# Kernel tuning notes

Hardware: AMD Instinct MI355X
Metric: run time of the kernel (lower is better)

The kernel has to match this reference:

```python
import jax, jax.numpy as jnp
from jax import lax
import numpy as np

THRESHOLD = 1.25
CURRENT_DECAY = 0.25
VOLTAGE_DECAY = 0.03
TAU_GRAD = 0.03
SCALE_GRAD = 3.0


@jax.custom_vjp
def spike_fn(v):
    # Heaviside spike on membrane voltage (threshold already subtracted)
    return (v >= 0.0).astype(v.dtype)

def _spike_fwd(v):
    return spike_fn(v), v

def _spike_bwd(v, g):
    # slayer-style exponential surrogate gradient around threshold
    surrogate = SCALE_GRAD * jnp.exp(-jnp.abs(v) / TAU_GRAD)
    return (g * surrogate,)

spike_fn.defvjp(_spike_fwd, _spike_bwd)


def cuba_dense(x, v_w, g_w, delay):
    """x: [B, C_in, T] spikes -> [B, C_out, T] spikes.
    Weight-normalized dense synapse + CUBA leaky-integrate-and-fire scan + axonal delay."""
    # weight norm: W = g * v / ||v||_row
    norm = jnp.sqrt(jnp.sum(v_w * v_w, axis=1, keepdims=True))
    W = g_w[:, None] * v_w / norm                       # [O, C]
    z = jnp.einsum('bct,oc->bot', x, W)                 # synaptic current input [B, O, T]
    B, O, T = z.shape
    zT = jnp.transpose(z, (2, 0, 1))                    # [T, B, O]

    def step(carry, zt):
        cur, vol = carry
        cur = cur * (1.0 - CURRENT_DECAY) + zt
        vol = vol * (1.0 - VOLTAGE_DECAY) + cur
        s = spike_fn(vol - THRESHOLD)
        vol = vol * (1.0 - s)                           # reset to zero on spike
        return (cur, vol), s

    init = (jnp.zeros((B, O), z.dtype), jnp.zeros((B, O), z.dtype))
    _, sT = lax.scan(step, init, zT)                    # [T, B, O]
    s = jnp.transpose(sT, (1, 2, 0))                    # [B, O, T]

    # per-neuron integer axonal delay: out[b,n,t] = s[b,n,t-d_n]
    t_idx = jnp.arange(T)[None, :] - delay[:, None]     # [O, T]
    valid = (t_idx >= 0)
    gathered = s[:, jnp.arange(O)[:, None], jnp.clip(t_idx, 0, T - 1)]
    return jnp.where(valid[None, :, :], gathered, jnp.zeros((), s.dtype))


def setup_inputs() -> dict:
    key = jax.random.key(0)
    ks = jax.random.split(key, 10)
    B, C, T = 32, 34 * 34 * 2, 300
    spike = (jax.random.uniform(ks[0], (B, C, T)) < 0.1).astype(jnp.float32)
    v1 = jax.random.normal(ks[1], (512, C), jnp.float32) * 0.1
    g1 = jax.random.uniform(ks[2], (512,), jnp.float32) + 0.5
    v2 = jax.random.normal(ks[3], (512, 512), jnp.float32) * 0.1
    g2 = jax.random.uniform(ks[4], (512,), jnp.float32) + 0.5
    v3 = jax.random.normal(ks[5], (10, 512), jnp.float32) * 0.1
    g3 = jax.random.uniform(ks[6], (10,), jnp.float32) + 0.5
    d1 = jax.random.randint(ks[7], (512,), 0, 8, jnp.int32)
    d2 = jax.random.randint(ks[8], (512,), 0, 8, jnp.int32)
    d3 = jax.random.randint(ks[9], (10,), 0, 8, jnp.int32)
    return {"spike": spike, "v1": v1, "g1": g1, "v2": v2, "g2": g2,
            "v3": v3, "g3": g3, "d1": d1, "d2": d2, "d3": d3}


def reference(spike, v1, g1, v2, g2, v3, g3, d1, d2, d3):
    s1 = cuba_dense(spike, v1, g1, d1)
    s2 = cuba_dense(s1, v2, g2, d2)
    s3 = cuba_dense(s2, v3, g3, d3)
    counts = jnp.stack([jnp.mean(s1), jnp.mean(s2), jnp.mean(s3)]).reshape(1, -1)
    return s3, counts
```

## Files before the change

### kernel.cpp

```cpp
#include <hip/hip_runtime.h>

#define B_   32
#define T_   300
#define C1_  2312
#define O1_  512
#define O2_  512
#define O3_  10
#define M_   (B_*T_)
#define KSPLIT_ 1152


__global__ void calc_f(const float* __restrict__ v, const float* __restrict__ g,
                       double* __restrict__ f, int O, int C) {
    int o = blockIdx.x;
    const float* row = v + (size_t)o * C;
    double s = 0.0;
    for (int c = threadIdx.x; c < C; c += blockDim.x) {
        double x = (double)row[c];
        s += x * x;
    }
    for (int off = 32; off; off >>= 1) s += __shfl_down(s, off);
    __shared__ double wsum[4];
    int lane = threadIdx.x & 63, wv = threadIdx.x >> 6;
    if (lane == 0) wsum[wv] = s;
    __syncthreads();
    if (threadIdx.x == 0) {
        double tot = 0.0;
        for (int i = 0; i < (int)(blockDim.x >> 6); ++i) tot += wsum[i];
        f[o] = (double)g[o] / sqrt(tot);
    }
}

__global__ void transpose_scale(const float* __restrict__ v, const double* __restrict__ f,
                                double* __restrict__ wt, int O, int C, int ldo) {
    __shared__ double tile[32][33];
    int c0 = blockIdx.x * 32, o0 = blockIdx.y * 32;
    int tx = threadIdx.x, ty = threadIdx.y;
    for (int k = 0; k < 4; ++k) {
        int o = o0 + ty + k * 8, c = c0 + tx;
        double val = 0.0;
        if (o < O && c < C) val = (double)v[(size_t)o * C + c] * f[o];
        tile[ty + k * 8][tx] = val;
    }
    __syncthreads();
    for (int k = 0; k < 4; ++k) {
        int c = c0 + ty + k * 8, o = o0 + tx;
        if (c < C && o < O) wt[(size_t)c * ldo + o] = tile[tx][ty + k * 8];
    }
}

__global__ void build_bits(const float* __restrict__ X, unsigned* __restrict__ bits) {
    size_t idx = (size_t)blockIdx.x * 256 + threadIdx.x;
    if (idx >= (size_t)B_ * C1_ * 10) return;
    int t32 = (int)(idx % 10);
    size_t bc = idx / 10;
    const float* src = X + bc * T_ + t32 * 32;
    int nq = (t32 == 9) ? 3 : 8;
    unsigned m = 0;
    for (int q = 0; q < nq; ++q) {
        float4 v = *(const float4*)(src + q * 4);
        if (v.x != 0.f) m |= 1u << (q * 4 + 0);
        if (v.y != 0.f) m |= 1u << (q * 4 + 1);
        if (v.z != 0.f) m |= 1u << (q * 4 + 2);
        if (v.w != 0.f) m |= 1u << (q * 4 + 3);
    }
    bits[idx] = m;
}

__global__ __launch_bounds__(512, 4) void gemm1(const unsigned* __restrict__ Xbits,
                                                const double* __restrict__ Wt,
                                                double* __restrict__ Z) {
    __shared__ double Ws[16][256];
    int n = blockIdx.x;
    int combo = n & 3;
    int khalf = combo & 1;
    int o0 = (combo >> 1) * 256;
    int i = n >> 2;
    int tb = i % 10;
    int bpair = i / 10;
    int tid = threadIdx.x;
    int w = tid >> 6;
    int lane = tid & 63;
    int b = bpair * 2 + (w >> 2);
    int w8s = __builtin_amdgcn_readfirstlane((w & 3) << 3);
    int cbeg = khalf ? KSPLIT_ : 0;
    const int NT = khalf ? 73 : 72;
    double acc[8][4];
#pragma unroll
    for (int tj = 0; tj < 8; ++tj)
#pragma unroll
        for (int i2 = 0; i2 < 4; ++i2) acc[tj][i2] = 0.0;
    const unsigned* xbp = Xbits + (size_t)b * C1_ * 10 + tb;

    double2 wreg[4];
    unsigned mval, mvaln = 0u;

    auto load_w = [&](int c0) {
#pragma unroll
        for (int h = 0; h < 4; ++h) {
            int idx = h * 512 + tid;
            int r = idx >> 7, od = (idx & 127) * 2;
            int c = c0 + r;
            double2 val; val.x = 0.0; val.y = 0.0;
            if (c < C1_) val = *(const double2*)(Wt + (size_t)c * O1_ + o0 + od);
            wreg[h] = val;
        }
    };
    auto load_m = [&](int c0) -> unsigned {
        int c = c0 + lane;
        return (lane < 16 && c < C1_) ? xbp[(size_t)c * 10] : 0u;
    };
    auto store_w = [&]() {
#pragma unroll
        for (int h = 0; h < 4; ++h) {
            int idx = h * 512 + tid;
            int r = idx >> 7, od = (idx & 127) * 2;
            *(double2*)(&Ws[r][od]) = wreg[h];
        }
    };

    load_w(cbeg);
    mval = load_m(cbeg);
    for (int tile = 0; tile < NT; ++tile) {
        store_w();
        __syncthreads();
        if (tile + 1 < NT) {
            int cn = cbeg + (tile + 1) * 16;
            load_w(cn);
            mvaln = load_m(cn);
        }
#pragma unroll
        for (int k = 0; k < 16; ++k) {
            unsigned smk = (unsigned)__builtin_amdgcn_readlane((int)mval, k);
            unsigned soct = (smk >> w8s) & 0xffu;
            if (soct) {
                double wf[4];
#pragma unroll
                for (int i2 = 0; i2 < 4; ++i2) wf[i2] = Ws[k][lane + 64 * i2];
#pragma unroll
                for (int tj = 0; tj < 8; ++tj) {
                    if (soct & (1u << tj)) {
#pragma unroll
                        for (int i2 = 0; i2 < 4; ++i2) acc[tj][i2] += wf[i2];
                    }
                }
            }
        }
        mval = mvaln;
        __syncthreads();
    }
#pragma unroll
    for (int tj = 0; tj < 8; ++tj) {
        int t = tb * 32 + w8s + tj;
        if (t < T_) {
            double* dst = Z + ((size_t)b * T_ + t) * O1_ + o0;
#pragma unroll
            for (int i2 = 0; i2 < 4; ++i2)
                atomicAdd(&dst[lane + 64 * i2], acc[tj][i2]);
        }
    }
}

__global__ __launch_bounds__(512, 4) void gemm2s(const unsigned* __restrict__ Sbits,
                                                 const double* __restrict__ Wt,
                                                 double* __restrict__ Z) {
    __shared__ double Ws[16][256];
    int n = blockIdx.x;
    int ohalf = n & 1;
    int o0 = ohalf * 256;
    int i = n >> 1;
    int twin = i % 5;
    int b = i / 5;
    int tid = threadIdx.x;
    int w = tid >> 6;
    int lane = tid & 63;
    int w8s = __builtin_amdgcn_readfirstlane((w & 3) << 3);
    int word = twin * 2 + (w >> 2);
    double acc[8][4];
#pragma unroll
    for (int tj = 0; tj < 8; ++tj)
#pragma unroll
        for (int i2 = 0; i2 < 4; ++i2) acc[tj][i2] = 0.0;
    const unsigned* xbp = Sbits + (size_t)b * O1_ * 10 + word;

    double2 wreg[4];
    unsigned mval, mvaln = 0u;

    auto load_w = [&](int c0) {
#pragma unroll
        for (int h = 0; h < 4; ++h) {
            int idx = h * 512 + tid;
            int r = idx >> 7, od = (idx & 127) * 2;
            int c = c0 + r;
            wreg[h] = *(const double2*)(Wt + (size_t)c * O2_ + o0 + od);
        }
    };
    auto load_m = [&](int c0) -> unsigned {
        int c = c0 + lane;
        return (lane < 16) ? xbp[(size_t)c * 10] : 0u;
    };
    auto store_w = [&]() {
#pragma unroll
        for (int h = 0; h < 4; ++h) {
            int idx = h * 512 + tid;
            int r = idx >> 7, od = (idx & 127) * 2;
            *(double2*)(&Ws[r][od]) = wreg[h];
        }
    };

    load_w(0);
    mval = load_m(0);
    for (int tile = 0; tile < 32; ++tile) {
        store_w();
        __syncthreads();
        if (tile + 1 < 32) {
            int cn = (tile + 1) * 16;
            load_w(cn);
            mvaln = load_m(cn);
        }
#pragma unroll
        for (int k = 0; k < 16; ++k) {
            unsigned smk = (unsigned)__builtin_amdgcn_readlane((int)mval, k);
            unsigned soct = (smk >> w8s) & 0xffu;
            if (soct) {
                double wf[4];
#pragma unroll
                for (int i2 = 0; i2 < 4; ++i2) wf[i2] = Ws[k][lane + 64 * i2];
#pragma unroll
                for (int tj = 0; tj < 8; ++tj) {
                    if (soct & (1u << tj)) {
#pragma unroll
                        for (int i2 = 0; i2 < 4; ++i2) acc[tj][i2] += wf[i2];
                    }
                }
            }
        }
        mval = mvaln;
        __syncthreads();
    }
#pragma unroll
    for (int tj = 0; tj < 8; ++tj) {
        int t = twin * 64 + w * 8 + tj;
        if (t < T_) {
            double* dst = Z + ((size_t)b * T_ + t) * O2_ + o0;
#pragma unroll
            for (int i2 = 0; i2 < 4; ++i2)
                dst[lane + 64 * i2] = acc[tj][i2];
        }
    }
}

__global__ void gemm3(const float* __restrict__ A,
                      const double* __restrict__ Wt,
                      double* __restrict__ Z) {
    __shared__ double w[512 * 16];
    for (int e = threadIdx.x; e < 4096; e += 256)
        ((double2*)w)[e] = ((const double2*)Wt)[e];
    __syncthreads();
    int m = blockIdx.x * 256 + threadIdx.x;
    if (m >= M_) return;
    double acc[O3_];
#pragma unroll
    for (int o = 0; o < O3_; ++o) acc[o] = 0.0;
    const float4* Ar = (const float4*)(A + (size_t)m * 512);
    for (int cq = 0; cq < 128; ++cq) {
        float4 a = Ar[cq];
        float av[4] = {a.x, a.y, a.z, a.w};
#pragma unroll
        for (int u = 0; u < 4; ++u)
#pragma unroll
            for (int o = 0; o < O3_; ++o) acc[o] += (double)av[u] * w[(cq * 4 + u) * 16 + o];
    }
    double* dst = Z + (size_t)m * 16;
#pragma unroll
    for (int o = 0; o < O3_; ++o) dst[o] = acc[o];
}

__global__ void scan12(const double* __restrict__ Zin,
                       const int* __restrict__ delay,
                       float* __restrict__ Sout,
                       unsigned* __restrict__ bitsOut,
                       float* __restrict__ sumOut) {
    int blk = blockIdx.x;
    int o = (blk & 7) * 64 + threadIdx.x;
    int b = blk >> 3;
    const double* z = Zin + (size_t)b * T_ * O1_ + o;
    float* s = Sout + (size_t)b * T_ * O1_ + o;
    unsigned* bp = bitsOut + ((size_t)b * O1_ + o) * 10;
    int d = delay[o];
    for (int t = 0; t < d; ++t) s[(size_t)t * O1_] = 0.f;
    double cur = 0.0, vol = 0.0;
    float cnt = 0.f;
    unsigned bw = 0u;
    for (int t8 = 0; t8 < 296; t8 += 8) {
        double zb[8];
#pragma unroll
        for (int u = 0; u < 8; ++u) zb[u] = z[(size_t)(t8 + u) * O1_];
#pragma unroll
        for (int u = 0; u < 8; ++u) {
            int t = t8 + u;
            cur = cur * 0.75 + zb[u];
            vol = vol * 0.97 + cur;
            float sp = (vol >= 1.25) ? 1.f : 0.f;
            if (sp > 0.f) vol = 0.0;
            int tw = t + d;
            if (tw < T_) {
                s[(size_t)tw * O1_] = sp; cnt += sp;
                if (sp > 0.f) bw |= 1u << (tw & 31);
                if ((tw & 31) == 31) { bp[tw >> 5] = bw; bw = 0u; }
            }
        }
    }
    {
        double zb[4];
#pragma unroll
        for (int u = 0; u < 4; ++u) zb[u] = z[(size_t)(296 + u) * O1_];
#pragma unroll
        for (int u = 0; u < 4; ++u) {
            int t = 296 + u;
            cur = cur * 0.75 + zb[u];
            vol = vol * 0.97 + cur;
            float sp = (vol >= 1.25) ? 1.f : 0.f;
            if (sp > 0.f) vol = 0.0;
            int tw = t + d;
            if (tw < T_) {
                s[(size_t)tw * O1_] = sp; cnt += sp;
                if (sp > 0.f) bw |= 1u << (tw & 31);
                if ((tw & 31) == 31) { bp[tw >> 5] = bw; bw = 0u; }
            }
        }
    }
    bp[9] = bw;
    for (int off = 32; off; off >>= 1) cnt += __shfl_down(cnt, off);
    if (threadIdx.x == 0) atomicAdd(sumOut, cnt);
}

__global__ void scan3(const double* __restrict__ Z3,
                      const int* __restrict__ d3,
                      float* __restrict__ out,
                      float* __restrict__ sumOut) {
    __shared__ double zt[T_ * 16];
    int b = blockIdx.x;
    const double2* src = (const double2*)(Z3 + (size_t)b * T_ * 16);
    for (int e = threadIdx.x; e < T_ * 8; e += 64)
        ((double2*)zt)[e] = src[e];
    __syncthreads();
    int o = threadIdx.x;
    if (o < O3_) {
        int d = d3[o];
        float* dst = out + (size_t)b * O3_ * T_ + (size_t)o * T_;
        for (int t = 0; t < d; ++t) dst[t] = 0.f;
        double cur = 0.0, vol = 0.0;
        float cnt = 0.f;
        for (int t = 0; t < T_; ++t) {
            cur = cur * 0.75 + zt[t * 16 + o];
            vol = vol * 0.97 + cur;
            float sp = (vol >= 1.25) ? 1.f : 0.f;
            if (sp > 0.f) vol = 0.0;
            int tw = t + d;
            if (tw < T_) { dst[tw] = sp; cnt += sp; }
        }
        atomicAdd(sumOut, cnt);
    }
}

__global__ void finalize(const float* __restrict__ sums, float* __restrict__ out) {
    if (threadIdx.x == 0) {
        out[0] = (float)((double)sums[0] / (double)(B_ * O1_ * T_));
        out[1] = (float)((double)sums[1] / (double)(B_ * O2_ * T_));
        out[2] = (float)((double)sums[2] / (double)(B_ * O3_ * T_));
    }
}

extern "C" void kernel_launch(void* const* d_in, const int* in_sizes, int n_in,
                              void* d_out, int out_size, void* d_ws, size_t ws_size,
                              hipStream_t stream) {
    const float* spike = (const float*)d_in[0];
    const float* v1 = (const float*)d_in[1];
    const float* g1 = (const float*)d_in[2];
    const float* v2 = (const float*)d_in[3];
    const float* g2 = (const float*)d_in[4];
    const float* v3 = (const float*)d_in[5];
    const float* g3 = (const float*)d_in[6];
    const int* d1 = (const int*)d_in[7];
    const int* d2 = (const int*)d_in[8];
    const int* d3 = (const int*)d_in[9];
    float* out = (float*)d_out;

    double* dw = (double*)d_ws;
    size_t off = 0;
    double* f1  = dw + off; off += 512;
    double* f2  = dw + off; off += 512;
    double* f3  = dw + off; off += 16;
    double* Wt1 = dw + off; off += (size_t)C1_ * O1_;
    double* Wt2 = dw + off; off += 512 * 512;
    double* Wt3 = dw + off; off += 512 * 16;
    double* zA  = dw + off; off += (size_t)M_ * 512;
    double* z3b = dw + off; off += (size_t)M_ * 16;
    float* fw = (float*)(dw + off);
    float* sB    = fw;
    float* sums  = fw + (size_t)M_ * 512;
    unsigned* Xbits = (unsigned*)(fw + (size_t)M_ * 512 + 4);
    unsigned* bits2 = Xbits + (size_t)B_ * C1_ * 10;
    (void)ws_size; (void)out_size; (void)in_sizes; (void)n_in;

    hipMemsetAsync(sums, 0, 4 * sizeof(float), stream);
    hipMemsetAsync(zA, 0, (size_t)M_ * 512 * sizeof(double), stream);

    build_bits<<<(B_ * C1_ * 10 + 255) / 256, 256, 0, stream>>>(spike, Xbits);

    calc_f<<<512, 256, 0, stream>>>(v1, g1, f1, O1_, C1_);
    calc_f<<<512, 256, 0, stream>>>(v2, g2, f2, O2_, O1_);
    calc_f<<<O3_, 256, 0, stream>>>(v3, g3, f3, O3_, O2_);

    transpose_scale<<<dim3((C1_ + 31) / 32, 16), dim3(32, 8), 0, stream>>>(v1, f1, Wt1, O1_, C1_, O1_);
    transpose_scale<<<dim3(16, 16), dim3(32, 8), 0, stream>>>(v2, f2, Wt2, O2_, O1_, O2_);
    transpose_scale<<<dim3(16, 1), dim3(32, 8), 0, stream>>>(v3, f3, Wt3, O3_, O2_, 16);

    gemm1<<<640, 512, 0, stream>>>(Xbits, Wt1, zA);
    scan12<<<256, 64, 0, stream>>>(zA, d1, sB, bits2, sums + 0);
    gemm2s<<<320, 512, 0, stream>>>(bits2, Wt2, zA);
    scan12<<<256, 64, 0, stream>>>(zA, d2, sB, bits2, sums + 1);
    gemm3<<<(M_ + 255) / 256, 256, 0, stream>>>(sB, Wt3, z3b);
    scan3<<<B_, 64, 0, stream>>>(z3b, d3, out, sums + 2);
    finalize<<<1, 64, 0, stream>>>(sums, out + (size_t)B_ * O3_ * T_);
}
```

Before: 854.3 us.

## Double-buffer GEMM weight tiles, split-K into separate buffers, drop atomics and memset

Both bit-sparse GEMMs now double-buffer the shared weight tile, which removes one barrier per K tile. gemm1 writes its two K halves to separate Z buffers with plain stores, replacing the atomicAdd and the 39 MB memset. gemm2s is also split along K across 640 blocks for more parallelism. scan12 sums the two partial buffers and skips the unneeded float spike output or bit output for each layer. In exchange it doubles shared memory per block, which may lower occupancy, adds an extra workspace buffer, and makes each scan read twice as much z data.

```diff
diff --git a/kernel.cpp b/kernel.cpp
--- a/kernel.cpp
+++ b/kernel.cpp
@@ -69,8 +69,9 @@
 
 __global__ __launch_bounds__(512, 4) void gemm1(const unsigned* __restrict__ Xbits,
                                                 const double* __restrict__ Wt,
-                                                double* __restrict__ Z) {
-    __shared__ double Ws[16][256];
+                                                double* __restrict__ Z0,
+                                                double* __restrict__ Z1) {
+    __shared__ double Ws[2][16][256];
     int n = blockIdx.x;
     int combo = n & 3;
     int khalf = combo & 1;
@@ -84,7 +85,9 @@
     int b = bpair * 2 + (w >> 2);
     int w8s = __builtin_amdgcn_readfirstlane((w & 3) << 3);
     int cbeg = khalf ? KSPLIT_ : 0;
+    int qend = khalf ? C1_ : KSPLIT_;
     const int NT = khalf ? 73 : 72;
+    double* __restrict__ Z = khalf ? Z1 : Z0;
     double acc[8][4];
 #pragma unroll
     for (int tj = 0; tj < 8; ++tj)
@@ -102,28 +105,29 @@
             int r = idx >> 7, od = (idx & 127) * 2;
             int c = c0 + r;
             double2 val; val.x = 0.0; val.y = 0.0;
-            if (c < C1_) val = *(const double2*)(Wt + (size_t)c * O1_ + o0 + od);
+            if (c < qend) val = *(const double2*)(Wt + (size_t)c * O1_ + o0 + od);
             wreg[h] = val;
         }
     };
     auto load_m = [&](int c0) -> unsigned {
         int c = c0 + lane;
-        return (lane < 16 && c < C1_) ? xbp[(size_t)c * 10] : 0u;
-    };
-    auto store_w = [&]() {
+        return (lane < 16 && c < qend) ? xbp[(size_t)c * 10] : 0u;
+    };
+    auto store_w = [&](int bi) {
 #pragma unroll
         for (int h = 0; h < 4; ++h) {
             int idx = h * 512 + tid;
             int r = idx >> 7, od = (idx & 127) * 2;
-            *(double2*)(&Ws[r][od]) = wreg[h];
+            *(double2*)(&Ws[bi][r][od]) = wreg[h];
         }
     };
 
     load_w(cbeg);
     mval = load_m(cbeg);
+    store_w(0);
+    __syncthreads();
+    int cur = 0;
     for (int tile = 0; tile < NT; ++tile) {
-        store_w();
-        __syncthreads();
         if (tile + 1 < NT) {
             int cn = cbeg + (tile + 1) * 16;
             load_w(cn);
@@ -136,7 +140,7 @@
             if (soct) {
                 double wf[4];
 #pragma unroll
-                for (int i2 = 0; i2 < 4; ++i2) wf[i2] = Ws[k][lane + 64 * i2];
+                for (int i2 = 0; i2 < 4; ++i2) wf[i2] = Ws[cur][k][lane + 64 * i2];
 #pragma unroll
                 for (int tj = 0; tj < 8; ++tj) {
                     if (soct & (1u << tj)) {
@@ -146,8 +150,12 @@
                 }
             }
         }
+        if (tile + 1 < NT) {
+            store_w(cur ^ 1);
+            __syncthreads();
+        }
         mval = mvaln;
-        __syncthreads();
+        cur ^= 1;
     }
 #pragma unroll
     for (int tj = 0; tj < 8; ++tj) {
@@ -156,19 +164,21 @@
             double* dst = Z + ((size_t)b * T_ + t) * O1_ + o0;
 #pragma unroll
             for (int i2 = 0; i2 < 4; ++i2)
-                atomicAdd(&dst[lane + 64 * i2], acc[tj][i2]);
+                dst[lane + 64 * i2] = acc[tj][i2];
         }
     }
 }
 
 __global__ __launch_bounds__(512, 4) void gemm2s(const unsigned* __restrict__ Sbits,
                                                  const double* __restrict__ Wt,
-                                                 double* __restrict__ Z) {
-    __shared__ double Ws[16][256];
+                                                 double* __restrict__ Z0,
+                                                 double* __restrict__ Z1) {
+    __shared__ double Ws[2][16][256];
     int n = blockIdx.x;
-    int ohalf = n & 1;
-    int o0 = ohalf * 256;
-    int i = n >> 1;
+    int combo = n & 3;
+    int khalf = combo & 1;
+    int o0 = (combo >> 1) * 256;
+    int i = n >> 2;
     int twin = i % 5;
     int b = i / 5;
     int tid = threadIdx.x;
@@ -176,6 +186,8 @@
     int lane = tid & 63;
     int w8s = __builtin_amdgcn_readfirstlane((w & 3) << 3);
     int word = twin * 2 + (w >> 2);
+    int cbeg = khalf * 256;
+    double* __restrict__ Z = khalf ? Z1 : Z0;
     double acc[8][4];
 #pragma unroll
     for (int tj = 0; tj < 8; ++tj)
@@ -199,22 +211,23 @@
         int c = c0 + lane;
         return (lane < 16) ? xbp[(size_t)c * 10] : 0u;
     };
-    auto store_w = [&]() {
+    auto store_w = [&](int bi) {
 #pragma unroll
         for (int h = 0; h < 4; ++h) {
             int idx = h * 512 + tid;
             int r = idx >> 7, od = (idx & 127) * 2;
-            *(double2*)(&Ws[r][od]) = wreg[h];
-        }
-    };
-
-    load_w(0);
-    mval = load_m(0);
-    for (int tile = 0; tile < 32; ++tile) {
-        store_w();
-        __syncthreads();
-        if (tile + 1 < 32) {
-            int cn = (tile + 1) * 16;
+            *(double2*)(&Ws[bi][r][od]) = wreg[h];
+        }
+    };
+
+    load_w(cbeg);
+    mval = load_m(cbeg);
+    store_w(0);
+    __syncthreads();
+    int cur = 0;
+    for (int tile = 0; tile < 16; ++tile) {
+        if (tile + 1 < 16) {
+            int cn = cbeg + (tile + 1) * 16;
             load_w(cn);
             mvaln = load_m(cn);
         }
@@ -225,7 +238,7 @@
             if (soct) {
                 double wf[4];
 #pragma unroll
-                for (int i2 = 0; i2 < 4; ++i2) wf[i2] = Ws[k][lane + 64 * i2];
+                for (int i2 = 0; i2 < 4; ++i2) wf[i2] = Ws[cur][k][lane + 64 * i2];
 #pragma unroll
                 for (int tj = 0; tj < 8; ++tj) {
                     if (soct & (1u << tj)) {
@@ -235,8 +248,12 @@
                 }
             }
         }
+        if (tile + 1 < 16) {
+            store_w(cur ^ 1);
+            __syncthreads();
+        }
         mval = mvaln;
-        __syncthreads();
+        cur ^= 1;
     }
 #pragma unroll
     for (int tj = 0; tj < 8; ++tj) {
@@ -276,7 +293,8 @@
     for (int o = 0; o < O3_; ++o) dst[o] = acc[o];
 }
 
-__global__ void scan12(const double* __restrict__ Zin,
+__global__ void scan12(const double* __restrict__ Za,
+                       const double* __restrict__ Zb,
                        const int* __restrict__ delay,
                        float* __restrict__ Sout,
                        unsigned* __restrict__ bitsOut,
@@ -284,53 +302,68 @@
     int blk = blockIdx.x;
     int o = (blk & 7) * 64 + threadIdx.x;
     int b = blk >> 3;
-    const double* z = Zin + (size_t)b * T_ * O1_ + o;
-    float* s = Sout + (size_t)b * T_ * O1_ + o;
-    unsigned* bp = bitsOut + ((size_t)b * O1_ + o) * 10;
+    size_t base = (size_t)b * T_ * O1_ + o;
+    const double* z  = Za + base;
+    const double* z2 = Zb ? Zb + base : nullptr;
+    float* s = Sout ? Sout + base : nullptr;
     int d = delay[o];
-    for (int t = 0; t < d; ++t) s[(size_t)t * O1_] = 0.f;
+    if (s) for (int t = 0; t < d; ++t) s[(size_t)t * O1_] = 0.f;
     double cur = 0.0, vol = 0.0;
     float cnt = 0.f;
     unsigned bw = 0u;
     for (int t8 = 0; t8 < 296; t8 += 8) {
-        double zb[8];
-#pragma unroll
-        for (int u = 0; u < 8; ++u) zb[u] = z[(size_t)(t8 + u) * O1_];
+        double zbuf[8];
+#pragma unroll
+        for (int u = 0; u < 8; ++u) zbuf[u] = z[(size_t)(t8 + u) * O1_];
+        if (z2) {
+#pragma unroll
+            for (int u = 0; u < 8; ++u) zbuf[u] += z2[(size_t)(t8 + u) * O1_];
+        }
 #pragma unroll
         for (int u = 0; u < 8; ++u) {
             int t = t8 + u;
-            cur = cur * 0.75 + zb[u];
+            cur = cur * 0.75 + zbuf[u];
             vol = vol * 0.97 + cur;
             float sp = (vol >= 1.25) ? 1.f : 0.f;
             if (sp > 0.f) vol = 0.0;
             int tw = t + d;
             if (tw < T_) {
-                s[(size_t)tw * O1_] = sp; cnt += sp;
-                if (sp > 0.f) bw |= 1u << (tw & 31);
-                if ((tw & 31) == 31) { bp[tw >> 5] = bw; bw = 0u; }
+                if (s) s[(size_t)tw * O1_] = sp;
+                cnt += sp;
+                if (bitsOut) {
+                    if (sp > 0.f) bw |= 1u << (tw & 31);
+                    if ((tw & 31) == 31) { bitsOut[((size_t)b * O1_ + o) * 10 + (tw >> 5)] = bw; bw = 0u; }
+                }
             }
         }
     }
     {
-        double zb[4];
-#pragma unroll
-        for (int u = 0; u < 4; ++u) zb[u] = z[(size_t)(296 + u) * O1_];
+        double zbuf[4];
+#pragma unroll
+        for (int u = 0; u < 4; ++u) zbuf[u] = z[(size_t)(296 + u) * O1_];
+        if (z2) {
+#pragma unroll
+            for (int u = 0; u < 4; ++u) zbuf[u] += z2[(size_t)(296 + u) * O1_];
+        }
 #pragma unroll
         for (int u = 0; u < 4; ++u) {
             int t = 296 + u;
-            cur = cur * 0.75 + zb[u];
+            cur = cur * 0.75 + zbuf[u];
             vol = vol * 0.97 + cur;
             float sp = (vol >= 1.25) ? 1.f : 0.f;
             if (sp > 0.f) vol = 0.0;
             int tw = t + d;
             if (tw < T_) {
-                s[(size_t)tw * O1_] = sp; cnt += sp;
-                if (sp > 0.f) bw |= 1u << (tw & 31);
-                if ((tw & 31) == 31) { bp[tw >> 5] = bw; bw = 0u; }
+                if (s) s[(size_t)tw * O1_] = sp;
+                cnt += sp;
+                if (bitsOut) {
+                    if (sp > 0.f) bw |= 1u << (tw & 31);
+                    if ((tw & 31) == 31) { bitsOut[((size_t)b * O1_ + o) * 10 + (tw >> 5)] = bw; bw = 0u; }
+                }
             }
         }
     }
-    bp[9] = bw;
+    if (bitsOut) bitsOut[((size_t)b * O1_ + o) * 10 + 9] = bw;
     for (int off = 32; off; off >>= 1) cnt += __shfl_down(cnt, off);
     if (threadIdx.x == 0) atomicAdd(sumOut, cnt);
 }
@@ -396,6 +429,7 @@
     double* Wt2 = dw + off; off += 512 * 512;
     double* Wt3 = dw + off; off += 512 * 16;
     double* zA  = dw + off; off += (size_t)M_ * 512;
+    double* zB  = dw + off; off += (size_t)M_ * 512;
     double* z3b = dw + off; off += (size_t)M_ * 16;
     float* fw = (float*)(dw + off);
     float* sB    = fw;
@@ -405,7 +439,6 @@
     (void)ws_size; (void)out_size; (void)in_sizes; (void)n_in;
 
     hipMemsetAsync(sums, 0, 4 * sizeof(float), stream);
-    hipMemsetAsync(zA, 0, (size_t)M_ * 512 * sizeof(double), stream);
 
     build_bits<<<(B_ * C1_ * 10 + 255) / 256, 256, 0, stream>>>(spike, Xbits);
 
@@ -417,10 +450,10 @@
     transpose_scale<<<dim3(16, 16), dim3(32, 8), 0, stream>>>(v2, f2, Wt2, O2_, O1_, O2_);
     transpose_scale<<<dim3(16, 1), dim3(32, 8), 0, stream>>>(v3, f3, Wt3, O3_, O2_, 16);
 
-    gemm1<<<640, 512, 0, stream>>>(Xbits, Wt1, zA);
-    scan12<<<256, 64, 0, stream>>>(zA, d1, sB, bits2, sums + 0);
-    gemm2s<<<320, 512, 0, stream>>>(bits2, Wt2, zA);
-    scan12<<<256, 64, 0, stream>>>(zA, d2, sB, bits2, sums + 1);
+    gemm1<<<640, 512, 0, stream>>>(Xbits, Wt1, zA, zB);
+    scan12<<<256, 64, 0, stream>>>(zA, zB, d1, nullptr, bits2, sums + 0);
+    gemm2s<<<640, 512, 0, stream>>>(bits2, Wt2, zA, zB);
+    scan12<<<256, 64, 0, stream>>>(zA, zB, d2, sB, nullptr, sums + 1);
     gemm3<<<(M_ + 255) / 256, 256, 0, stream>>>(sB, Wt3, z3b);
     scan3<<<B_, 64, 0, stream>>>(z3b, d3, out, sums + 2);
     finalize<<<1, 64, 0, stream>>>(sums, out + (size_t)B_ * O3_ * T_);
```

New measurement: 794.1 us. -7.0%, faster.
